# Optimization experiments

Hardware: AMD Instinct MI355X
Metric: run time of the kernel (lower is better)

The kernel has to match this reference:

```python
import jax, jax.numpy as jnp
import numpy as np

B, K, N, D = 8, 512, 16384, 128


def setup_inputs() -> dict:
    key = jax.random.key(0)
    k1, k2, k3, k4, k5 = jax.random.split(key, 5)
    return {
        "points": jax.random.normal(k1, (B, 3, N), dtype=jnp.float32),
        "src_embedding": jax.random.normal(k2, (B, D, N), dtype=jnp.float32),
        "tgt_embedding": jax.random.normal(k3, (B, D, N), dtype=jnp.float32),
        "temperature": jnp.ones((B,), dtype=jnp.float32),
        "conv_w": jax.random.normal(k4, (2 * D,), dtype=jnp.float32) * 0.02,
        "gumbel_noise": jax.random.uniform(k5, (B, K, N), dtype=jnp.float32),
    }


def reference(points, src_embedding, tgt_embedding, temperature, conv_w, gumbel_noise):
    b, _, n = points.shape
    # adaptive_max_pool1d to size 1 == global max over points
    tgt_global = jnp.max(tgt_embedding, axis=2, keepdims=True)          # [B,D,1]
    # Conv1d(2D,1,k=1,no bias) on cat([src, tgt_global_expanded]) splits into two dots
    d = src_embedding.shape[1]
    w_src, w_tgt = conv_w[:d], conv_w[d:]
    logits = (jnp.einsum('bdn,d->bn', src_embedding, w_src)
              + jnp.einsum('bdo,d->bo', tgt_global, w_tgt))              # [B,N] (tgt term broadcast)
    logits = logits[:, None, :]                                          # [B,1,N] -> broadcast over K
    # gumbel-softmax, hard=True
    eps = 1e-10
    u = jnp.clip(gumbel_noise, eps, 1.0 - eps)
    g = -jnp.log(-jnp.log(u))                                            # [B,K,N]
    tau = temperature[:, None, None]
    y_soft = jax.nn.softmax((logits + g) / tau, axis=-1)                 # [B,K,N]
    idx = jnp.argmax(y_soft, axis=-1)                                    # [B,K]
    y_hard = jax.nn.one_hot(idx, n, dtype=y_soft.dtype)
    scores = y_hard - jax.lax.stop_gradient(y_soft) + y_soft             # straight-through
    # matmul-as-gather: points @ scores^T, src_embedding @ scores^T
    new_points = jnp.einsum('bcn,bkn->bck', points, scores)              # [B,3,K]
    new_embedding = jnp.einsum('bdn,bkn->bdk', src_embedding, scores)    # [B,D,K]
    return (new_points, new_embedding)
```

## Files before the change

kernel.cpp:

```cpp
#include <hip/hip_runtime.h>
#include <math.h>

constexpr int B = 8, K = 512, N = 16384, D = 128;

constexpr int TQ = 256;

__global__ __launch_bounds__(256) void k_q(const float* __restrict__ src,
                                           const float* __restrict__ conv_w,
                                           const float* __restrict__ temp,
                                           float* __restrict__ q) {
    const int b  = blockIdx.x / (N / TQ);
    const int nb = blockIdx.x % (N / TQ);
    const int dg = threadIdx.x >> 6;
    const int ln = threadIdx.x & 63;
    const float* sp = src + (size_t)b * D * N + (size_t)nb * TQ + ln * 4;
    const int d0 = dg * 32;

    float4 acc = make_float4(0.f, 0.f, 0.f, 0.f);
#pragma unroll
    for (int t = 0; t < 4; ++t) {
        float4 v[8];
#pragma unroll
        for (int j = 0; j < 8; ++j)
            v[j] = *(const float4*)(sp + (size_t)(d0 + t * 8 + j) * N);
#pragma unroll
        for (int j = 0; j < 8; ++j) {
            const float w = conv_w[d0 + t * 8 + j];
            acc.x = fmaf(v[j].x, w, acc.x);
            acc.y = fmaf(v[j].y, w, acc.y);
            acc.z = fmaf(v[j].z, w, acc.z);
            acc.w = fmaf(v[j].w, w, acc.w);
        }
    }

    __shared__ float4 ps[4][64];
    ps[dg][ln] = acc;
    __syncthreads();
    if (dg == 0) {
        const float4 a0 = ps[0][ln], a1 = ps[1][ln], a2 = ps[2][ln], a3 = ps[3][ln];
        const float sgn = (temp[b] < 0.f) ? -1.f : 1.f;
        float4 o;
        o.x = sgn * expf(-(a0.x + a1.x + a2.x + a3.x));
        o.y = sgn * expf(-(a0.y + a1.y + a2.y + a3.y));
        o.z = sgn * expf(-(a0.z + a1.z + a2.z + a3.z));
        o.w = sgn * expf(-(a0.w + a1.w + a2.w + a3.w));
        ((float4*)(q + (size_t)b * N + (size_t)nb * TQ))[ln] = o;
    }
}

__device__ __forceinline__ float neg_ln(float u) {
    u = fmaxf(u, 1e-10f);
    const float w = 1.0f - u;
    const float tf = __builtin_amdgcn_logf(u) * -0.69314718056f;
    const float tp = w * fmaf(w, fmaf(w, 0.33333334f, 0.5f), 1.0f);
    return (w < 0.0078125f) ? tp : tf;
}

__device__ __forceinline__ void amin_update(float v, int n, float& best, int& bi) {
    if (v < best) { best = v; bi = n; }
}

__global__ __launch_bounds__(256) void k_argmin_gather(
    const float* __restrict__ gum, const float* __restrict__ q,
    const float* __restrict__ points, const float* __restrict__ src,
    float* __restrict__ out) {
    const int b = blockIdx.x / K;
    const int k = blockIdx.x % K;
    const float4* gp = (const float4*)(gum + (size_t)blockIdx.x * N);
    const float4* qp = (const float4*)(q + (size_t)b * N);

    float best = INFINITY;
    int bi = 0;
#pragma unroll
    for (int r4 = 0; r4 < 4; ++r4) {
        const int i0 = threadIdx.x + r4 * 4 * 256;
        float4 g[4], qv[4];
#pragma unroll
        for (int j = 0; j < 4; ++j) {
            g[j]  = gp[i0 + j * 256];
            qv[j] = qp[i0 + j * 256];
        }
#pragma unroll
        for (int j = 0; j < 4; ++j) {
            const int n0 = (i0 + j * 256) * 4;
            amin_update(neg_ln(g[j].x) * qv[j].x, n0 + 0, best, bi);
            amin_update(neg_ln(g[j].y) * qv[j].y, n0 + 1, best, bi);
            amin_update(neg_ln(g[j].z) * qv[j].z, n0 + 2, best, bi);
            amin_update(neg_ln(g[j].w) * qv[j].w, n0 + 3, best, bi);
        }
    }

    for (int off = 32; off; off >>= 1) {
        float ov = __shfl_down(best, off);
        int oi = __shfl_down(bi, off);
        if (ov < best || (ov == best && oi < bi)) { best = ov; bi = oi; }
    }
    __shared__ float sv[4];
    __shared__ int si[4];
    __shared__ int sidx;
    if ((threadIdx.x & 63) == 0) {
        sv[threadIdx.x >> 6] = best;
        si[threadIdx.x >> 6] = bi;
    }
    __syncthreads();
    if (threadIdx.x == 0) {
#pragma unroll
        for (int j = 1; j < 4; ++j) {
            if (sv[j] < best || (sv[j] == best && si[j] < bi)) { best = sv[j]; bi = si[j]; }
        }
        sidx = bi;
    }
    __syncthreads();

    const int row = threadIdx.x;
    if (row < 3 + D) {
        const int id = sidx;
        if (row < 3) {
            out[((size_t)b * 3 + row) * K + k] = points[((size_t)b * 3 + row) * N + id];
        } else {
            const int d = row - 3;
            out[(size_t)B * 3 * K + ((size_t)b * D + d) * K + k] =
                src[((size_t)b * D + d) * N + id];
        }
    }
}

extern "C" void kernel_launch(void* const* d_in, const int* in_sizes, int n_in,
                              void* d_out, int out_size, void* d_ws, size_t ws_size,
                              hipStream_t stream) {
    const float* points = (const float*)d_in[0];
    const float* src    = (const float*)d_in[1];
    const float* temp   = (const float*)d_in[3];
    const float* conv_w = (const float*)d_in[4];
    const float* gum    = (const float*)d_in[5];
    float* out = (float*)d_out;

    float* q = (float*)d_ws;

    k_q<<<B * (N / TQ), 256, 0, stream>>>(src, conv_w, temp, q);
    k_argmin_gather<<<B * K, 256, 0, stream>>>(gum, q, points, src, out);
}
```

Before: 434.7 us.

## Process eight K rows per block reusing q held in registers

Each block now handles eight gumbel rows for the same batch instead of one. The q row is loaded into registers once and reused across all eight rows, which cuts redundant q reads from cache or memory. The trade-off is fewer blocks (512 instead of 4096), serialized rows with two syncs each, and 64 extra VGPRs for q, which may reduce occupancy and latency hiding on a kernel dominated by streaming the gumbel noise.

```diff
diff --git a/kernel.cpp b/kernel.cpp
--- a/kernel.cpp
+++ b/kernel.cpp
@@ -48,6 +48,9 @@
     }
 }
 
+constexpr int R = 8;
+constexpr int GROUPS = K / R;
+
 __device__ __forceinline__ float neg_ln(float u) {
     u = fmaxf(u, 1e-10f);
     const float w = 1.0f - u;
@@ -64,63 +67,73 @@
     const float* __restrict__ gum, const float* __restrict__ q,
     const float* __restrict__ points, const float* __restrict__ src,
     float* __restrict__ out) {
-    const int b = blockIdx.x / K;
-    const int k = blockIdx.x % K;
-    const float4* gp = (const float4*)(gum + (size_t)blockIdx.x * N);
+    const int b  = blockIdx.x / GROUPS;
+    const int kg = blockIdx.x % GROUPS;
+    const int k0 = kg * R;
     const float4* qp = (const float4*)(q + (size_t)b * N);
 
-    float best = INFINITY;
-    int bi = 0;
+    float4 qreg[16];
 #pragma unroll
-    for (int r4 = 0; r4 < 4; ++r4) {
-        const int i0 = threadIdx.x + r4 * 4 * 256;
-        float4 g[4], qv[4];
-#pragma unroll
-        for (int j = 0; j < 4; ++j) {
-            g[j]  = gp[i0 + j * 256];
-            qv[j] = qp[i0 + j * 256];
-        }
-#pragma unroll
-        for (int j = 0; j < 4; ++j) {
-            const int n0 = (i0 + j * 256) * 4;
-            amin_update(neg_ln(g[j].x) * qv[j].x, n0 + 0, best, bi);
-            amin_update(neg_ln(g[j].y) * qv[j].y, n0 + 1, best, bi);
-            amin_update(neg_ln(g[j].z) * qv[j].z, n0 + 2, best, bi);
-            amin_update(neg_ln(g[j].w) * qv[j].w, n0 + 3, best, bi);
-        }
-    }
+    for (int j = 0; j < 16; ++j) qreg[j] = qp[threadIdx.x + j * 256];
 
-    for (int off = 32; off; off >>= 1) {
-        float ov = __shfl_down(best, off);
-        int oi = __shfl_down(bi, off);
-        if (ov < best || (ov == best && oi < bi)) { best = ov; bi = oi; }
-    }
     __shared__ float sv[4];
     __shared__ int si[4];
-    __shared__ int sidx;
-    if ((threadIdx.x & 63) == 0) {
-        sv[threadIdx.x >> 6] = best;
-        si[threadIdx.x >> 6] = bi;
+    __shared__ int sidxs[R];
+
+    for (int r = 0; r < R; ++r) {
+        const float4* gp = (const float4*)(gum + ((size_t)(b * K + k0 + r)) * N);
+        float best = INFINITY;
+        int bi = 0;
+#pragma unroll
+        for (int r4 = 0; r4 < 4; ++r4) {
+            const int i0 = threadIdx.x + r4 * 4 * 256;
+            float4 g[4];
+#pragma unroll
+            for (int j = 0; j < 4; ++j) g[j] = gp[i0 + j * 256];
+#pragma unroll
+            for (int j = 0; j < 4; ++j) {
+                const float4 qv = qreg[r4 * 4 + j];
+                const int n0 = (i0 + j * 256) * 4;
+                amin_update(neg_ln(g[j].x) * qv.x, n0 + 0, best, bi);
+                amin_update(neg_ln(g[j].y) * qv.y, n0 + 1, best, bi);
+                amin_update(neg_ln(g[j].z) * qv.z, n0 + 2, best, bi);
+                amin_update(neg_ln(g[j].w) * qv.w, n0 + 3, best, bi);
+            }
+        }
+
+        for (int off = 32; off; off >>= 1) {
+            float ov = __shfl_down(best, off);
+            int oi = __shfl_down(bi, off);
+            if (ov < best || (ov == best && oi < bi)) { best = ov; bi = oi; }
+        }
+        if ((threadIdx.x & 63) == 0) {
+            sv[threadIdx.x >> 6] = best;
+            si[threadIdx.x >> 6] = bi;
+        }
+        __syncthreads();
+        if (threadIdx.x == 0) {
+#pragma unroll
+            for (int j = 1; j < 4; ++j) {
+                if (sv[j] < best || (sv[j] == best && si[j] < bi)) { best = sv[j]; bi = si[j]; }
+            }
+            sidxs[r] = bi;
+        }
+        __syncthreads();
     }
-    __syncthreads();
-    if (threadIdx.x == 0) {
-#pragma unroll
-        for (int j = 1; j < 4; ++j) {
-            if (sv[j] < best || (sv[j] == best && si[j] < bi)) { best = sv[j]; bi = si[j]; }
-        }
-        sidx = bi;
-    }
-    __syncthreads();
 
     const int row = threadIdx.x;
     if (row < 3 + D) {
-        const int id = sidx;
-        if (row < 3) {
-            out[((size_t)b * 3 + row) * K + k] = points[((size_t)b * 3 + row) * N + id];
-        } else {
-            const int d = row - 3;
-            out[(size_t)B * 3 * K + ((size_t)b * D + d) * K + k] =
-                src[((size_t)b * D + d) * N + id];
+#pragma unroll
+        for (int r = 0; r < R; ++r) {
+            const int id = sidxs[r];
+            const int k = k0 + r;
+            if (row < 3) {
+                out[((size_t)b * 3 + row) * K + k] = points[((size_t)b * 3 + row) * N + id];
+            } else {
+                const int d = row - 3;
+                out[(size_t)B * 3 * K + ((size_t)b * D + d) * K + k] =
+                    src[((size_t)b * D + d) * N + id];
+            }
         }
     }
 }
@@ -138,5 +151,5 @@
     float* q = (float*)d_ws;
 
     k_q<<<B * (N / TQ), 256, 0, stream>>>(src, conv_w, temp, q);
-    k_argmin_gather<<<B * K, 256, 0, stream>>>(gum, q, points, src, out);
+    k_argmin_gather<<<B * GROUPS, 256, 0, stream>>>(gum, q, points, src, out);
 }
```

New measurement: 437.0 us, median of 2. Within noise of the previous version (+0.5%).
